# Kernel tuning notes

Measured on AMD Instinct MI355X. Metric: run time of the kernel, lower is better.

## Reference

```python
import jax, jax.numpy as jnp
import numpy as np

N, D_IN, D_OUT = 128, 512, 512
B = 256

def setup_inputs() -> dict:
    key = jax.random.key(0)
    kx, kw, kb = jax.random.split(key, 3)
    x = jax.random.normal(kx, (B, N, D_IN), dtype=jnp.float32)
    # nn.Linear default init: uniform(-1/sqrt(d_in), 1/sqrt(d_in)) for weight and bias
    bound = 1.0 / np.sqrt(D_IN)
    weight = jax.random.uniform(kw, (N, D_IN, D_OUT), dtype=jnp.float32, minval=-bound, maxval=bound)
    bias = jax.random.uniform(kb, (N, D_OUT), dtype=jnp.float32, minval=-bound, maxval=bound)
    return {"x": x, "weight": weight, "bias": bias}

def reference(x, weight, bias):
    # per-position linear: out[b,n,o] = sum_i x[b,n,i] * W[n,i,o] + bias[n,o]
    out = jnp.einsum('bni,nio->bno', x, weight)
    return out + bias[None]
```

## Files before the change

kernel.cpp:

```cpp
#include <hip/hip_runtime.h>

typedef __attribute__((ext_vector_type(8))) __bf16 bf16x8;
typedef __attribute__((ext_vector_type(4))) float f32x4;

#define DI   512
#define DO   512
#define XROW (128 * DI)
#define OROW (128 * DO)
#define BK   32

#define VMCNT(n) asm volatile("s_waitcnt vmcnt(" #n ")" ::: "memory")
#define LGKM0()  asm volatile("s_waitcnt lgkmcnt(0)" ::: "memory")
#define SBAR()   __builtin_amdgcn_s_barrier()
#define SCHED0() __builtin_amdgcn_sched_barrier(0)


__global__ __launch_bounds__(512, 4)
void nlinear_mfma(const float* __restrict__ xp, const float* __restrict__ wp,
                  const float* __restrict__ bp, float* __restrict__ op) {
  int blk = blockIdx.x;
  int L  = ((blk & 7) << 7) + (blk >> 3);
  int n  = L >> 3;
  int mt = (L >> 2) & 1;
  int ot = L & 3;
  int mBase = mt << 7;
  int oBase = ot << 7;

  __shared__ float  aT[2][128 * BK];
  __shared__ __bf16 bT[2][128 * BK];

  int tid  = threadIdx.x;
  int wid  = tid >> 6;
  int lane = tid & 63;
  int wm  = (wid >> 2) << 6;
  int wn  = (wid & 3) << 5;
  int l16 = lane & 15;
  int l4  = lane >> 4;

  unsigned aOff[2];
  #pragma unroll
  for (int i = 0; i < 2; ++i) {
    int r0  = (wid << 4) + (i << 3);
    int row = r0 + (lane >> 3);
    int g   = (lane & 7) ^ ((row >> 1) & 7);
    aOff[i] = (unsigned)(((mBase + row) * XROW + n * DI) * 4 + g * 16);
  }

  int bo   = (tid & 63) + (((tid >> 6) & 1) << 6);
  int bks  = (tid >> 7) & 3;
  unsigned bOff = (unsigned)((((unsigned)n * DI + (bks << 3)) * DO + oBase + bo) * 4);
  int bWslot = bks ^ ((bo >> 1) & 3);

  float bReg[8];
  auto loadB = [&](int kt) {
    #pragma unroll
    for (int r = 0; r < 8; ++r)
      bReg[r] = *(const float*)((const char*)wp + bOff + (unsigned)(kt * BK + r) * (DO * 4));
  };
  auto writeB = [&](int buf) {
    bf16x8 v;
    #pragma unroll
    for (int r = 0; r < 8; ++r)
      v[r] = (__bf16)bReg[r];
    *(bf16x8*)((char*)bT[buf] + bo * 64 + bWslot * 16) = v;
  };
  auto gloadA = [&](int buf, int kt) {
    #pragma unroll
    for (int i = 0; i < 2; ++i) {
      int r0 = (wid << 4) + (i << 3);
      __builtin_amdgcn_global_load_lds(
          (const __attribute__((address_space(1))) void*)
              ((const char*)xp + aOff[i] + (unsigned)(kt * 128)),
          (__attribute__((address_space(3))) void*)((char*)aT[buf] + r0 * 128),
          16, 0, 0);
    }
  };

  f32x4 acc[4][2];
  #pragma unroll
  for (int i = 0; i < 4; ++i)
    #pragma unroll
    for (int j = 0; j < 2; ++j)
      acc[i][j] = f32x4{0.f, 0.f, 0.f, 0.f};

  auto compute = [&](int buf) {
    bf16x8 bfr[2];
    #pragma unroll
    for (int j = 0; j < 2; ++j) {
      int row  = wn + j * 16 + l16;
      int slot = l4 ^ ((row >> 1) & 3);
      bfr[j] = *(const bf16x8*)((const char*)bT[buf] + row * 64 + slot * 16);
    }
    #pragma unroll
    for (int i = 0; i < 4; ++i) {
      int row = wm + i * 16 + l16;
      int v7  = (row >> 1) & 7;
      const char* rb = (const char*)aT[buf] + row * 128;
      f32x4 lo = *(const f32x4*)(rb + (((2 * l4)     ^ v7) * 16));
      f32x4 hi = *(const f32x4*)(rb + (((2 * l4 + 1) ^ v7) * 16));
      bf16x8 a;
      a[0] = (__bf16)lo.x; a[1] = (__bf16)lo.y; a[2] = (__bf16)lo.z; a[3] = (__bf16)lo.w;
      a[4] = (__bf16)hi.x; a[5] = (__bf16)hi.y; a[6] = (__bf16)hi.z; a[7] = (__bf16)hi.w;
      acc[i][0] = __builtin_amdgcn_mfma_f32_16x16x32_bf16(a, bfr[0], acc[i][0], 0, 0, 0);
      acc[i][1] = __builtin_amdgcn_mfma_f32_16x16x32_bf16(a, bfr[1], acc[i][1], 0, 0, 0);
    }
  };

  float bi[2];
  #pragma unroll
  for (int j = 0; j < 2; ++j)
    bi[j] = bp[n * DO + oBase + wn + j * 16 + l16];

  loadB(0);
  gloadA(0, 0);
  writeB(0);
  loadB(1);
  gloadA(1, 1);
  SCHED0();
  VMCNT(10);
  LGKM0();
  SBAR();
  SCHED0();

  for (int kt = 0; kt < 16; ++kt) {
    int cur = kt & 1;
    compute(cur);
    if (kt < 15) {
      SBAR();
      SCHED0();
      writeB(cur ^ 1);
      if (kt < 14) {
        loadB(kt + 2);
        gloadA(cur, kt + 2);
        SCHED0();
        VMCNT(10);
      } else {
        SCHED0();
        VMCNT(0);
      }
      LGKM0();
      SBAR();
      SCHED0();
    }
  }

  #pragma unroll
  for (int i = 0; i < 4; ++i) {
    #pragma unroll
    for (int j = 0; j < 2; ++j) {
      #pragma unroll
      for (int r = 0; r < 4; ++r) {
        int m = mBase + wm + i * 16 + l4 * 4 + r;
        int o = oBase + wn + j * 16 + l16;
        op[(size_t)m * OROW + n * DO + o] = acc[i][j][r] + bi[j];
      }
    }
  }
}

extern "C" void kernel_launch(void* const* d_in, const int* in_sizes, int n_in,
                              void* d_out, int out_size, void* d_ws, size_t ws_size,
                              hipStream_t stream) {
  const float* x = (const float*)d_in[0];
  const float* w = (const float*)d_in[1];
  const float* b = (const float*)d_in[2];
  float* o = (float*)d_out;
  hipLaunchKernelGGL(nlinear_mfma, dim3(1024), dim3(512), 0, stream, x, w, b, o);
}
```

Baseline: 53.82 us.

## Convert A to bf16 in registers before LDS, double BK, restructure pipeline

Drops the direct global-to-LDS fp32 load of the activation tile. A is now loaded into registers and converted to bf16 before it is stored in shared memory, so it is converted once per tile rather than on every fragment read. The K tile grows from 32 to 64 with an XOR swizzle shared by A and B, which halves the number of iterations and barriers. The main loop now writes the next buffer before computing the current one, with a single barrier per iteration. In exchange the A tile goes through VGPRs, adding register pressure, and the loop relies on compiler-inserted waits instead of explicit vmcnt control.

```diff
diff --git a/kernel.cpp b/kernel.cpp
--- a/kernel.cpp
+++ b/kernel.cpp
@@ -2,18 +2,22 @@
 
 typedef __attribute__((ext_vector_type(8))) __bf16 bf16x8;
 typedef __attribute__((ext_vector_type(4))) float f32x4;
+typedef __attribute__((ext_vector_type(2))) float f32x2;
 
 #define DI   512
 #define DO   512
 #define XROW (128 * DI)
 #define OROW (128 * DO)
-#define BK   32
+#define BK   64
+#define NT   8
 
-#define VMCNT(n) asm volatile("s_waitcnt vmcnt(" #n ")" ::: "memory")
 #define LGKM0()  asm volatile("s_waitcnt lgkmcnt(0)" ::: "memory")
 #define SBAR()   __builtin_amdgcn_s_barrier()
 #define SCHED0() __builtin_amdgcn_sched_barrier(0)
 
+__device__ __forceinline__ int swz(int row, int kbyte) {
+  return (row * 128 + kbyte) ^ ((row & 7) << 4);
+}
 
 __global__ __launch_bounds__(512, 4)
 void nlinear_mfma(const float* __restrict__ xp, const float* __restrict__ wp,
@@ -26,53 +30,56 @@
   int mBase = mt << 7;
   int oBase = ot << 7;
 
-  __shared__ float  aT[2][128 * BK];
+  __shared__ __bf16 aT[2][128 * BK];
   __shared__ __bf16 bT[2][128 * BK];
 
   int tid  = threadIdx.x;
+  int lane = tid & 63;
   int wid  = tid >> 6;
-  int lane = tid & 63;
   int wm  = (wid >> 2) << 6;
   int wn  = (wid & 3) << 5;
   int l16 = lane & 15;
   int l4  = lane >> 4;
 
-  unsigned aOff[2];
-  #pragma unroll
-  for (int i = 0; i < 2; ++i) {
-    int r0  = (wid << 4) + (i << 3);
-    int row = r0 + (lane >> 3);
-    int g   = (lane & 7) ^ ((row >> 1) & 7);
-    aOff[i] = (unsigned)(((mBase + row) * XROW + n * DI) * 4 + g * 16);
-  }
+  int am  = tid >> 2;
+  int akc = (tid & 3) << 4;
+  const float* aSrc = xp + (size_t)(mBase + am) * XROW + n * DI + akc;
 
-  int bo   = (tid & 63) + (((tid >> 6) & 1) << 6);
-  int bks  = (tid >> 7) & 3;
-  unsigned bOff = (unsigned)((((unsigned)n * DI + (bks << 3)) * DO + oBase + bo) * 4);
-  int bWslot = bks ^ ((bo >> 1) & 3);
+  int bo2 = (tid & 63) << 1;
+  int bkq = tid >> 6;
+  const float* bSrc = wp + ((size_t)n * DI + (bkq << 3)) * DO + oBase + bo2;
 
-  float bReg[8];
+  f32x4 aS[4];
+  f32x2 bS[8];
+
+  auto loadA = [&](int kt) {
+    #pragma unroll
+    for (int i = 0; i < 4; ++i)
+      aS[i] = *(const f32x4*)(aSrc + kt * BK + i * 4);
+  };
   auto loadB = [&](int kt) {
     #pragma unroll
-    for (int r = 0; r < 8; ++r)
-      bReg[r] = *(const float*)((const char*)wp + bOff + (unsigned)(kt * BK + r) * (DO * 4));
+    for (int j = 0; j < 8; ++j)
+      bS[j] = *(const f32x2*)(bSrc + (size_t)(kt * BK + j) * DO);
+  };
+  auto writeA = [&](int buf) {
+    #pragma unroll
+    for (int h = 0; h < 2; ++h) {
+      bf16x8 v;
+      #pragma unroll
+      for (int e = 0; e < 8; ++e)
+        v[e] = (__bf16)aS[h * 2 + (e >> 2)][e & 3];
+      *(bf16x8*)((char*)aT[buf] + swz(am, (akc + h * 8) * 2)) = v;
+    }
   };
   auto writeB = [&](int buf) {
-    bf16x8 v;
     #pragma unroll
-    for (int r = 0; r < 8; ++r)
-      v[r] = (__bf16)bReg[r];
-    *(bf16x8*)((char*)bT[buf] + bo * 64 + bWslot * 16) = v;
-  };
-  auto gloadA = [&](int buf, int kt) {
-    #pragma unroll
-    for (int i = 0; i < 2; ++i) {
-      int r0 = (wid << 4) + (i << 3);
-      __builtin_amdgcn_global_load_lds(
-          (const __attribute__((address_space(1))) void*)
-              ((const char*)xp + aOff[i] + (unsigned)(kt * 128)),
-          (__attribute__((address_space(3))) void*)((char*)aT[buf] + r0 * 128),
-          16, 0, 0);
+    for (int p = 0; p < 2; ++p) {
+      bf16x8 v;
+      #pragma unroll
+      for (int j = 0; j < 8; ++j)
+        v[j] = (__bf16)(p ? bS[j].y : bS[j].x);
+      *(bf16x8*)((char*)bT[buf] + swz(bo2 + p, bkq * 16)) = v;
     }
   };
 
@@ -84,25 +91,22 @@
       acc[i][j] = f32x4{0.f, 0.f, 0.f, 0.f};
 
   auto compute = [&](int buf) {
-    bf16x8 bfr[2];
     #pragma unroll
-    for (int j = 0; j < 2; ++j) {
-      int row  = wn + j * 16 + l16;
-      int slot = l4 ^ ((row >> 1) & 3);
-      bfr[j] = *(const bf16x8*)((const char*)bT[buf] + row * 64 + slot * 16);
-    }
-    #pragma unroll
-    for (int i = 0; i < 4; ++i) {
-      int row = wm + i * 16 + l16;
-      int v7  = (row >> 1) & 7;
-      const char* rb = (const char*)aT[buf] + row * 128;
-      f32x4 lo = *(const f32x4*)(rb + (((2 * l4)     ^ v7) * 16));
-      f32x4 hi = *(const f32x4*)(rb + (((2 * l4 + 1) ^ v7) * 16));
-      bf16x8 a;
-      a[0] = (__bf16)lo.x; a[1] = (__bf16)lo.y; a[2] = (__bf16)lo.z; a[3] = (__bf16)lo.w;
-      a[4] = (__bf16)hi.x; a[5] = (__bf16)hi.y; a[6] = (__bf16)hi.z; a[7] = (__bf16)hi.w;
-      acc[i][0] = __builtin_amdgcn_mfma_f32_16x16x32_bf16(a, bfr[0], acc[i][0], 0, 0, 0);
-      acc[i][1] = __builtin_amdgcn_mfma_f32_16x16x32_bf16(a, bfr[1], acc[i][1], 0, 0, 0);
+    for (int ks = 0; ks < 2; ++ks) {
+      bf16x8 af[4], bfr[2];
+      #pragma unroll
+      for (int i = 0; i < 4; ++i)
+        af[i] = *(const bf16x8*)((const char*)aT[buf] +
+                                 swz(wm + i * 16 + l16, ks * 64 + l4 * 16));
+      #pragma unroll
+      for (int j = 0; j < 2; ++j)
+        bfr[j] = *(const bf16x8*)((const char*)bT[buf] +
+                                  swz(wn + j * 16 + l16, ks * 64 + l4 * 16));
+      #pragma unroll
+      for (int i = 0; i < 4; ++i) {
+        acc[i][0] = __builtin_amdgcn_mfma_f32_16x16x32_bf16(af[i], bfr[0], acc[i][0], 0, 0, 0);
+        acc[i][1] = __builtin_amdgcn_mfma_f32_16x16x32_bf16(af[i], bfr[1], acc[i][1], 0, 0, 0);
+      }
     }
   };
 
@@ -111,36 +115,28 @@
   for (int j = 0; j < 2; ++j)
     bi[j] = bp[n * DO + oBase + wn + j * 16 + l16];
 
-  loadB(0);
-  gloadA(0, 0);
-  writeB(0);
-  loadB(1);
-  gloadA(1, 1);
+  loadA(0); loadB(0);
+  writeA(0); writeB(0);
+  loadA(1); loadB(1);
   SCHED0();
-  VMCNT(10);
   LGKM0();
   SBAR();
-  SCHED0();
 
-  for (int kt = 0; kt < 16; ++kt) {
+  for (int kt = 0; kt < NT; ++kt) {
     int cur = kt & 1;
+    int nxt = cur ^ 1;
+    if (kt + 1 < NT) {
+      writeA(nxt);
+      if (kt + 2 < NT) loadA(kt + 2);
+      writeB(nxt);
+      if (kt + 2 < NT) loadB(kt + 2);
+      SCHED0();
+    }
     compute(cur);
-    if (kt < 15) {
-      SBAR();
+    if (kt + 1 < NT) {
       SCHED0();
-      writeB(cur ^ 1);
-      if (kt < 14) {
-        loadB(kt + 2);
-        gloadA(cur, kt + 2);
-        SCHED0();
-        VMCNT(10);
-      } else {
-        SCHED0();
-        VMCNT(0);
-      }
       LGKM0();
       SBAR();
-      SCHED0();
     }
   }
 
```

Measured after the change: 73.94 us. +37.4%, slower.
